# Kernel tuning notes

Hardware: AMD Instinct MI355X
Metric: run time of the kernel (lower is better)

## Reference

```python
import jax, jax.numpy as jnp
import numpy as np

B, T, C = 4, 1024, 768
H, HS = 12, 64           # num_heads, head_size
VD = 2 * HS              # value dim per head


def setup_inputs() -> dict:
    key = jax.random.key(0)
    ks = jax.random.split(key, 16)
    s = 0.02
    inp = {
        "x": jax.random.normal(ks[0], (B, T, C), jnp.float32),
        "Wq1": jax.random.normal(ks[1], (H, C, HS), jnp.float32) * s,
        "Wk1": jax.random.normal(ks[2], (H, C, HS), jnp.float32) * s,
        "Wq2": jax.random.normal(ks[3], (H, C, HS), jnp.float32) * s,
        "Wk2": jax.random.normal(ks[4], (H, C, HS), jnp.float32) * s,
        "Wv": jax.random.normal(ks[5], (H, C, VD), jnp.float32) * s,
        "lq1": jax.random.normal(ks[6], (H, HS), jnp.float32) * 0.1,
        "lk1": jax.random.normal(ks[7], (H, HS), jnp.float32) * 0.1,
        "lq2": jax.random.normal(ks[8], (H, HS), jnp.float32) * 0.1,
        "lk2": jax.random.normal(ks[9], (H, HS), jnp.float32) * 0.1,
        "gn_w": jnp.ones((H * VD,), jnp.float32),
        "gn_b": jnp.zeros((H * VD,), jnp.float32),
        "Wp": jax.random.normal(ks[10], (C, H * VD), jnp.float32) * s,
        "bp": jnp.zeros((C,), jnp.float32),
        "layer_idx": 3,
    }
    return inp


def _diff_attn(x, Wq1, Wk1, Wq2, Wk2, Wv, lq1, lk1, lq2, lk2,
               gn_w, gn_b, Wp, bp, layer_idx):
    Bc, Tc, _ = x.shape
    scale = 1.0 / jnp.sqrt(jnp.float32(HS))
    # per-head projections: [B,H,T,HS]
    q1 = jnp.einsum('btc,hcd->bhtd', x, Wq1)
    k1 = jnp.einsum('btc,hcd->bhtd', x, Wk1)
    q2 = jnp.einsum('btc,hcd->bhtd', x, Wq2)
    k2 = jnp.einsum('btc,hcd->bhtd', x, Wk2)
    v = jnp.einsum('btc,hce->bhte', x, Wv)           # [B,H,T,2HS]
    mask = jnp.tril(jnp.ones((Tc, Tc), bool))         # causal
    neg = jnp.float32(-jnp.inf)
    a1 = jnp.einsum('bhtd,bhsd->bhts', q1, k1) * scale
    a2 = jnp.einsum('bhtd,bhsd->bhts', q2, k2) * scale
    a1 = jax.nn.softmax(jnp.where(mask, a1, neg), axis=-1)
    a2 = jax.nn.softmax(jnp.where(mask, a2, neg), axis=-1)
    # dynamic lambda init, per get_lambda
    li = jnp.float32(layer_idx)
    dyn = 0.8 - 0.6 * jnp.exp(-0.3 * (li - 1.0))
    lam = jnp.mean(jnp.exp(lq1 * lk1) - jnp.exp(lq2 * lk2) + dyn, axis=-1)  # [H]
    diff = a1 - lam[None, :, None, None] * a2
    out = jnp.einsum('bhts,bhse->bhte', diff, v)      # [B,H,T,2HS]
    out = out.transpose(0, 2, 1, 3).reshape(Bc, Tc, H * VD)
    # GroupLayerNorm == full layernorm over last dim (unbiased=False var)
    mu = out.mean(-1, keepdims=True)
    var = jnp.mean((out - mu) ** 2, axis=-1, keepdims=True)
    out = (out - mu) / jnp.sqrt(var + 1e-5) * gn_w + gn_b
    out = out * 0.2  # (1 - lambda_init_buffer=0.8), buffer never updated
    return out @ Wp.T + bp


def reference(x, Wq1, Wk1, Wq2, Wk2, Wv, lq1, lk1, lq2, lk2,
              gn_w, gn_b, Wp, bp, layer_idx):
    return _diff_attn(x, Wq1, Wk1, Wq2, Wk2, Wv, lq1, lk1, lq2, lk2,
                      gn_w, gn_b, Wp, bp, layer_idx)
```

## Files before the change

### kernel.cpp

```cpp
#include <hip/hip_runtime.h>
#include <hip/hip_bf16.h>

#define Bc   4
#define Tc   1024
#define Cc   768
#define Hc   12
#define HSc  64
#define VDc  128
#define NQKV 4608
#define YLD  3072
#define NROWS 4096
#define HVD  1536

#define Q1OFF 0
#define K1OFF 768
#define Q2OFF 1536
#define K2OFF 2304

typedef __bf16 bf16x8 __attribute__((ext_vector_type(8)));
typedef float f32x4 __attribute__((ext_vector_type(4)));
typedef unsigned int u32x4 __attribute__((ext_vector_type(4)));

#define EXP2SCALE 0.18033688011112042f

static __device__ __forceinline__ float bf2f(unsigned short s) {
    return __uint_as_float(((unsigned int)s) << 16);
}
static __device__ __forceinline__ unsigned short f2bf(float f) {
    unsigned int u = __float_as_uint(f);
    unsigned int r = (u + 0x7FFFu + ((u >> 16) & 1u)) >> 16;
    return (unsigned short)r;
}
static __device__ __forceinline__ unsigned int pack2bf(float lo, float hi) {
    unsigned int a = (__float_as_uint(lo) + 0x8000u) >> 16;
    unsigned int b = (__float_as_uint(hi) + 0x8000u) & 0xFFFF0000u;
    return a | b;
}
static __device__ __forceinline__ float fast_exp2(float x) {
    float r;
    asm("v_exp_f32 %0, %1" : "=v"(r) : "v"(x));
    return r;
}

static __device__ __forceinline__ void load16_lds(const void* g, void* l) {
    __builtin_amdgcn_global_load_lds(
        (const __attribute__((address_space(1))) void*)g,
        (__attribute__((address_space(3))) void*)l, 16, 0, 0);
}

__global__ __launch_bounds__(256) void cast_bf16(
    const float* __restrict__ src, unsigned short* __restrict__ dst)
{
    int i = blockIdx.x * 256 + threadIdx.x;
    float4 v = *(const float4*)(src + (size_t)i * 4);
    ushort4 u;
    u.x = f2bf(v.x); u.y = f2bf(v.y); u.z = f2bf(v.z); u.w = f2bf(v.w);
    *(ushort4*)(dst + (size_t)i * 4) = u;
}

__global__ __launch_bounds__(256) void trans_w(
    const float* __restrict__ Wq1, const float* __restrict__ Wk1,
    const float* __restrict__ Wq2, const float* __restrict__ Wk2,
    const float* __restrict__ Wv, unsigned short* __restrict__ WcatT)
{
    __shared__ float tile[64][65];
    int tid = threadIdx.x;
    int t = blockIdx.x;
    int kt = t % 12, nt = t / 12;
    int k0 = kt * 64, n0 = nt * 64;
    const float* src;
    int stride;
    if (n0 < 3072) {
        int which = n0 / 768, m = n0 - which * 768, h = m >> 6;
        const float* W = (which == 0) ? Wq1 : (which == 1) ? Wk1 : (which == 2) ? Wq2 : Wk2;
        src = W + ((size_t)h * 768 + k0) * 64;
        stride = 64;
    } else {
        int rel = n0 - 3072, h = rel >> 7, e0 = rel & 127;
        src = Wv + ((size_t)h * 768 + k0) * 128 + e0;
        stride = 128;
    }
    for (int i = tid; i < 4096; i += 256) {
        int kl = i >> 6, dl = i & 63;
        tile[dl][kl] = src[(size_t)kl * stride + dl];
    }
    __syncthreads();
    for (int i = tid; i < 4096; i += 256) {
        int nl = i >> 6, kl = i & 63;
        WcatT[(size_t)(n0 + nl) * 768 + k0 + kl] = f2bf(tile[nl][kl]);
    }
}

__global__ __launch_bounds__(64) void lambda_kernel(
    const float* __restrict__ lq1, const float* __restrict__ lk1,
    const float* __restrict__ lq2, const float* __restrict__ lk2,
    const int* __restrict__ layer_idx, float* __restrict__ lam)
{
    int h = blockIdx.x, l = threadIdx.x;
    float li = (float)layer_idx[0];
    float dyn = 0.8f - 0.6f * expf(-0.3f * (li - 1.0f));
    int i = h * HSc + l;
    float v = expf(lq1[i] * lk1[i]) - expf(lq2[i] * lk2[i]) + dyn;
    #pragma unroll
    for (int off = 32; off; off >>= 1) v += __shfl_xor(v, off);
    if (l == 0) lam[h] = v * (1.0f / 64.0f);
}

template<int TN, int KD, int LDC, bool OUT_BIAS, bool SPLITV>
__global__ __launch_bounds__(256) void gemm_mfma(
    const unsigned short* __restrict__ A, const unsigned short* __restrict__ Bt,
    unsigned short* __restrict__ Cb, float* __restrict__ Cf,
    const float* __restrict__ bias, unsigned short* __restrict__ VtOut)
{
    constexpr int BN = TN * 32;
    constexpr int JB = TN / 2;
    __shared__ unsigned short As[128 * 32];
    __shared__ unsigned short Bs[BN * 32];
    int tid = threadIdx.x, lane = tid & 63, w = tid >> 6;
    int wm = w >> 1, wn = w & 1;
    int m0 = blockIdx.y * 128, n0 = blockIdx.x * BN;

    int lr = lane >> 2, lq = lane & 3;
    const unsigned short* gA[2];
    const unsigned short* gB[JB];
    #pragma unroll
    for (int j = 0; j < 2; ++j) {
        int row = w * 32 + j * 16 + lr;
        int qg = lq ^ ((row >> 1) & 3);
        gA[j] = A + (size_t)(m0 + row) * KD + qg * 8;
    }
    #pragma unroll
    for (int j = 0; j < JB; ++j) {
        int row = w * (JB * 16) + j * 16 + lr;
        int qg = lq ^ ((row >> 1) & 3);
        gB[j] = Bt + (size_t)(n0 + row) * KD + qg * 8;
    }

    int rr = lane & 15, qd = lane >> 4;
    const unsigned short* aAddr[4];
    const unsigned short* bAddr[TN];
    #pragma unroll
    for (int i = 0; i < 4; ++i) {
        int row = wm * 64 + i * 16 + rr;
        int qs = qd ^ ((row >> 1) & 3);
        aAddr[i] = As + row * 32 + qs * 8;
    }
    #pragma unroll
    for (int t = 0; t < TN; ++t) {
        int row = wn * (TN * 16) + t * 16 + rr;
        int qs = qd ^ ((row >> 1) & 3);
        bAddr[t] = Bs + row * 32 + qs * 8;
    }

    f32x4 acc[4][TN];
    #pragma unroll
    for (int i = 0; i < 4; ++i)
        #pragma unroll
        for (int t = 0; t < TN; ++t) acc[i][t] = {0.f, 0.f, 0.f, 0.f};

    for (int k = 0; k < KD / 32; ++k) {
        __syncthreads();
        load16_lds(gA[0], As + (w * 2 + 0) * 512);
        load16_lds(gA[1], As + (w * 2 + 1) * 512);
        #pragma unroll
        for (int j = 0; j < JB; ++j)
            load16_lds(gB[j], Bs + (w * JB + j) * 512);
        gA[0] += 32; gA[1] += 32;
        #pragma unroll
        for (int j = 0; j < JB; ++j) gB[j] += 32;
        __syncthreads();

        bf16x8 af[4], bfr[TN];
        #pragma unroll
        for (int i = 0; i < 4; ++i) af[i] = *(const bf16x8*)aAddr[i];
        #pragma unroll
        for (int t = 0; t < TN; ++t) bfr[t] = *(const bf16x8*)bAddr[t];
        #pragma unroll
        for (int i = 0; i < 4; ++i)
            #pragma unroll
            for (int t = 0; t < TN; ++t)
                acc[i][t] = __builtin_amdgcn_mfma_f32_16x16x32_bf16(af[i], bfr[t], acc[i][t], 0, 0, 0);
    }

    #pragma unroll
    for (int t = 0; t < TN; ++t) {
        int col = n0 + wn * (TN * 16) + t * 16 + rr;
        if (SPLITV && col >= 3072) {
            int rel = col - 3072, hh = rel >> 7, e = rel & 127;
            #pragma unroll
            for (int i = 0; i < 4; ++i) {
                int row0 = m0 + wm * 64 + i * 16 + qd * 4;
                int b = row0 >> 10, tt = row0 & 1023;
                ushort4 pk;
                pk.x = f2bf(acc[i][t][0]); pk.y = f2bf(acc[i][t][1]);
                pk.z = f2bf(acc[i][t][2]); pk.w = f2bf(acc[i][t][3]);
                *(ushort4*)&VtOut[(size_t)((b * Hc + hh) * 128 + e) * 1024 + tt] = pk;
            }
        } else {
            float bv = OUT_BIAS ? bias[col] : 0.f;
            #pragma unroll
            for (int i = 0; i < 4; ++i) {
                #pragma unroll
                for (int r = 0; r < 4; ++r) {
                    int row = m0 + wm * 64 + i * 16 + qd * 4 + r;
                    if (OUT_BIAS)
                        Cf[(size_t)row * LDC + col] = acc[i][t][r] + bv;
                    else
                        Cb[(size_t)row * LDC + col] = f2bf(acc[i][t][r]);
                }
            }
        }
    }
}

__global__ __launch_bounds__(256) void diff_attn_mfma(
    const unsigned short* __restrict__ Y, const unsigned short* __restrict__ Vt,
    const float* __restrict__ lam_buf, unsigned short* __restrict__ attn)
{
    __shared__ __align__(16) unsigned short KVring[3 * 8192];

    int bh = blockIdx.x;
    int b = bh / Hc, h = bh - b * Hc;
    int g = 15 - (int)blockIdx.y;
    int tid = threadIdx.x, lane = tid & 63, wv = tid >> 6;
    int cl = lane & 15, qd = lane >> 4;
    float lamv = lam_buf[h];
    size_t rowbase = (size_t)(b * Tc) * YLD;
    const int hq = h * HSc;
    const unsigned short* VtB = Vt + ((size_t)bh << 17);
    const f32x4 zero4 = {0.f, 0.f, 0.f, 0.f};

    int ksrow = lane >> 3;
    int ksch  = (lane & 7) ^ ksrow;
    int offk[4];
    {
        int mat = wv & 1;
        int moff = mat ? K2OFF : K1OFF;
        #pragma unroll
        for (int r8 = 0; r8 < 4; ++r8)
            offk[r8] = (r8 * 8 + ksrow) * YLD + moff + hq + ksch * 8;
    }
    int vsel = lane >> 2;
    int vsch = (lane & 3) ^ ((vsel >> 1) & 3);
    int offv[4];
    {
        int sv0 = (wv & 1) * 4;
        #pragma unroll
        for (int i = 0; i < 4; ++i)
            offv[i] = ((sv0 + i) * 16 + vsel) * 1024 + vsch * 8;
    }

    auto stage = [&](int kt, int slot) {
        char* base = (char*)KVring + slot * 16384 + wv * 4096;
        if (wv < 2) {
            const unsigned short* g0 = Y + rowbase + (size_t)(kt * 32) * YLD;
            #pragma unroll
            for (int r8 = 0; r8 < 4; ++r8)
                load16_lds(g0 + offk[r8], base + r8 * 1024);
        } else {
            const unsigned short* g0 = VtB + kt * 32;
            #pragma unroll
            for (int i = 0; i < 4; ++i)
                load16_lds(g0 + offv[i], base + i * 1024);
        }
    };

    int kfo[2][4], vfo[8];
    #pragma unroll
    for (int c = 0; c < 2; ++c) {
        int row = c * 16 + cl;
        #pragma unroll
        for (int j = 0; j < 4; ++j)
            kfo[c][j] = (j >> 1) * 4096 + row * 128 +
                        ((((j & 1) * 4 + qd) ^ (row & 7)) << 4);
    }
    #pragma unroll
    for (int ec = 0; ec < 8; ++ec) {
        int e = ec * 16 + cl;
        vfo[ec] = 8192 + e * 64 + ((qd ^ ((e >> 1) & 3)) << 4);
    }

    int idxA = ((32 * (qd & 1)) + cl) * 4;
    int idxB = idxA + 64;
    bool loHalf = (qd < 2);

    int qrow = g * 64 + wv * 16;

    size_t qoff = rowbase + (size_t)(qrow + cl) * YLD;
    u32x4 uq1a = *(const u32x4*)(Y + qoff + Q1OFF + hq + qd * 8);
    u32x4 uq1b = *(const u32x4*)(Y + qoff + Q1OFF + hq + 32 + qd * 8);
    u32x4 uq2a = *(const u32x4*)(Y + qoff + Q2OFF + hq + qd * 8);
    u32x4 uq2b = *(const u32x4*)(Y + qoff + Q2OFF + hq + 32 + qd * 8);
    asm volatile("" : "+v"(uq1a), "+v"(uq1b), "+v"(uq2a), "+v"(uq2b));
    asm volatile("" : "+v"(lamv));
    asm volatile("s_waitcnt vmcnt(0)" ::: "memory");
    bf16x8 q1a = __builtin_bit_cast(bf16x8, uq1a);
    bf16x8 q1b = __builtin_bit_cast(bf16x8, uq1b);
    bf16x8 q2a = __builtin_bit_cast(bf16x8, uq2a);
    bf16x8 q2b = __builtin_bit_cast(bf16x8, uq2b);

    f32x4 O1[8], O2[8];
    #pragma unroll
    for (int ec = 0; ec < 8; ++ec) { O1[ec] = zero4; O2[ec] = zero4; }
    float l1s = 0.f, l2s = 0.f;

    int NT = 2 * g + 2;
    int ktmax = 2 * g + (wv >> 1);

    stage(0, 0);
    stage(1, 1);

    int cur = 0;
    for (int kt = 0; kt < NT; ++kt) {
        if (kt < NT - 1) {
            asm volatile("s_waitcnt vmcnt(4)\n\ts_barrier" ::: "memory");
        } else {
            asm volatile("s_waitcnt vmcnt(0)\n\ts_barrier" ::: "memory");
        }
        const char* kb = (const char*)KVring + cur * 16384;

        bf16x8 kf[2][4];
        #pragma unroll
        for (int c = 0; c < 2; ++c)
            #pragma unroll
            for (int j = 0; j < 4; ++j)
                kf[c][j] = *(const bf16x8*)(kb + kfo[c][j]);
        bf16x8 vf[8];
        #pragma unroll
        for (int ec = 0; ec < 8; ++ec)
            vf[ec] = *(const bf16x8*)(kb + vfo[ec]);

        if (kt + 2 < NT) {
            int st = cur + 2; if (st >= 3) st -= 3;
            stage(kt + 2, st);
        }

        if (kt <= ktmax) {
            f32x4 S1[2], S2[2];
            #pragma unroll
            for (int c = 0; c < 2; ++c) { S1[c] = zero4; S2[c] = zero4; }
            #pragma unroll
            for (int c = 0; c < 2; ++c) {
                S1[c] = __builtin_amdgcn_mfma_f32_16x16x32_bf16(kf[c][0], q1a, S1[c], 0, 0, 0);
                S1[c] = __builtin_amdgcn_mfma_f32_16x16x32_bf16(kf[c][1], q1b, S1[c], 0, 0, 0);
                S2[c] = __builtin_amdgcn_mfma_f32_16x16x32_bf16(kf[c][2], q2a, S2[c], 0, 0, 0);
                S2[c] = __builtin_amdgcn_mfma_f32_16x16x32_bf16(kf[c][3], q2b, S2[c], 0, 0, 0);
            }
            if (kt * 32 + 31 > qrow) {
                #pragma unroll
                for (int c = 0; c < 2; ++c) {
                    int lim = qrow + cl - kt * 32 - c * 16 - qd * 4;
                    #pragma unroll
                    for (int r = 0; r < 4; ++r) {
                        if (r > lim) { S1[c][r] = -1e30f; S2[c][r] = -1e30f; }
                    }
                }
            }
            float p1v[2][4], p2v[2][4];
            #pragma unroll
            for (int c = 0; c < 2; ++c) {
                #pragma unroll
                for (int r = 0; r < 4; ++r) {
                    p1v[c][r] = fast_exp2(S1[c][r] * EXP2SCALE);
                    p2v[c][r] = fast_exp2(S2[c][r] * EXP2SCALE);
                    l1s += p1v[c][r];
                    l2s += p2v[c][r];
                }
            }
            unsigned int s1m[2][2], s2m[2][2];
            #pragma unroll
            for (int c = 0; c < 2; ++c) {
                s1m[c][0] = pack2bf(p1v[c][0], p1v[c][1]);
                s1m[c][1] = pack2bf(p1v[c][2], p1v[c][3]);
                s2m[c][0] = pack2bf(p2v[c][0], p2v[c][1]);
                s2m[c][1] = pack2bf(p2v[c][2], p2v[c][3]);
            }
            u32x4 U1, U2;
            {
                int a00 = __builtin_amdgcn_ds_bpermute(idxA, (int)s1m[0][0]);
                int a10 = __builtin_amdgcn_ds_bpermute(idxA, (int)s1m[1][0]);
                int a01 = __builtin_amdgcn_ds_bpermute(idxA, (int)s1m[0][1]);
                int a11 = __builtin_amdgcn_ds_bpermute(idxA, (int)s1m[1][1]);
                int b00 = __builtin_amdgcn_ds_bpermute(idxB, (int)s1m[0][0]);
                int b10 = __builtin_amdgcn_ds_bpermute(idxB, (int)s1m[1][0]);
                int b01 = __builtin_amdgcn_ds_bpermute(idxB, (int)s1m[0][1]);
                int b11 = __builtin_amdgcn_ds_bpermute(idxB, (int)s1m[1][1]);
                U1[0] = (unsigned)(loHalf ? a00 : a10);
                U1[1] = (unsigned)(loHalf ? a01 : a11);
                U1[2] = (unsigned)(loHalf ? b00 : b10);
                U1[3] = (unsigned)(loHalf ? b01 : b11);
            }
            {
                int a00 = __builtin_amdgcn_ds_bpermute(idxA, (int)s2m[0][0]);
                int a10 = __builtin_amdgcn_ds_bpermute(idxA, (int)s2m[1][0]);
                int a01 = __builtin_amdgcn_ds_bpermute(idxA, (int)s2m[0][1]);
                int a11 = __builtin_amdgcn_ds_bpermute(idxA, (int)s2m[1][1]);
                int b00 = __builtin_amdgcn_ds_bpermute(idxB, (int)s2m[0][0]);
                int b10 = __builtin_amdgcn_ds_bpermute(idxB, (int)s2m[1][0]);
                int b01 = __builtin_amdgcn_ds_bpermute(idxB, (int)s2m[0][1]);
                int b11 = __builtin_amdgcn_ds_bpermute(idxB, (int)s2m[1][1]);
                U2[0] = (unsigned)(loHalf ? a00 : a10);
                U2[1] = (unsigned)(loHalf ? a01 : a11);
                U2[2] = (unsigned)(loHalf ? b00 : b10);
                U2[3] = (unsigned)(loHalf ? b01 : b11);
            }
            bf16x8 pa1 = __builtin_bit_cast(bf16x8, U1);
            bf16x8 pa2 = __builtin_bit_cast(bf16x8, U2);
            #pragma unroll
            for (int ec = 0; ec < 8; ++ec) {
                O1[ec] = __builtin_amdgcn_mfma_f32_16x16x32_bf16(pa1, vf[ec], O1[ec], 0, 0, 0);
                O2[ec] = __builtin_amdgcn_mfma_f32_16x16x32_bf16(pa2, vf[ec], O2[ec], 0, 0, 0);
            }
        }
        cur = (cur == 2) ? 0 : cur + 1;
    }

    l1s += __shfl_xor(l1s, 16); l1s += __shfl_xor(l1s, 32);
    l2s += __shfl_xor(l2s, 16); l2s += __shfl_xor(l2s, 32);
    float w1[4], w2[4];
    #pragma unroll
    for (int r = 0; r < 4; ++r) {
        float d1 = __shfl(l1s, qd * 4 + r);
        float d2 = __shfl(l2s, qd * 4 + r);
        w1[r] = 1.0f / d1;
        w2[r] = lamv / d2;
    }
    #pragma unroll
    for (int ec = 0; ec < 8; ++ec) {
        #pragma unroll
        for (int r = 0; r < 4; ++r) {
            size_t row = (size_t)(b * Tc + qrow + qd * 4 + r);
            attn[row * HVD + h * VDc + ec * 16 + cl] =
                f2bf(O1[ec][r] * w1[r] - O2[ec][r] * w2[r]);
        }
    }
}

__global__ __launch_bounds__(128) void ln_inplace(
    unsigned short* __restrict__ attn,
    const float* __restrict__ gnw, const float* __restrict__ gnb)
{
    int row = blockIdx.x, tid = threadIdx.x;
    unsigned short* p = attn + (size_t)row * HVD;
    float v[12];
    float s = 0.f, sq = 0.f;
    #pragma unroll
    for (int j = 0; j < 3; ++j) {
        int g = tid + j * 128;
        ushort4 u = *(const ushort4*)(p + g * 4);
        float x0 = bf2f(u.x), x1 = bf2f(u.y), x2 = bf2f(u.z), x3 = bf2f(u.w);
        v[j * 4 + 0] = x0; v[j * 4 + 1] = x1; v[j * 4 + 2] = x2; v[j * 4 + 3] = x3;
        s += x0 + x1 + x2 + x3;
        sq = fmaf(x0, x0, sq); sq = fmaf(x1, x1, sq);
        sq = fmaf(x2, x2, sq); sq = fmaf(x3, x3, sq);
    }
    #pragma unroll
    for (int off = 32; off; off >>= 1) { s += __shfl_xor(s, off); sq += __shfl_xor(sq, off); }
    __shared__ float ss[2], sqs[2];
    if ((tid & 63) == 0) { ss[tid >> 6] = s; sqs[tid >> 6] = sq; }
    __syncthreads();
    float S = ss[0] + ss[1], Q = sqs[0] + sqs[1];
    float mu = S * (1.0f / HVD);
    float rstd = rsqrtf(Q * (1.0f / HVD) - mu * mu + 1e-5f);
    #pragma unroll
    for (int j = 0; j < 3; ++j) {
        int g = tid + j * 128;
        float4 gw = *(const float4*)(gnw + g * 4);
        float4 gb = *(const float4*)(gnb + g * 4);
        ushort4 o;
        o.x = f2bf(((v[j * 4 + 0] - mu) * rstd * gw.x + gb.x) * 0.2f);
        o.y = f2bf(((v[j * 4 + 1] - mu) * rstd * gw.y + gb.y) * 0.2f);
        o.z = f2bf(((v[j * 4 + 2] - mu) * rstd * gw.z + gb.z) * 0.2f);
        o.w = f2bf(((v[j * 4 + 3] - mu) * rstd * gw.w + gb.w) * 0.2f);
        *(ushort4*)(p + g * 4) = o;
    }
}

extern "C" void kernel_launch(void* const* d_in, const int* in_sizes, int n_in,
                              void* d_out, int out_size, void* d_ws, size_t ws_size,
                              hipStream_t stream)
{
    const float* x   = (const float*)d_in[0];
    const float* Wq1 = (const float*)d_in[1];
    const float* Wk1 = (const float*)d_in[2];
    const float* Wq2 = (const float*)d_in[3];
    const float* Wk2 = (const float*)d_in[4];
    const float* Wv  = (const float*)d_in[5];
    const float* lq1 = (const float*)d_in[6];
    const float* lk1 = (const float*)d_in[7];
    const float* lq2 = (const float*)d_in[8];
    const float* lk2 = (const float*)d_in[9];
    const float* gnw = (const float*)d_in[10];
    const float* gnb = (const float*)d_in[11];
    const float* Wp  = (const float*)d_in[12];
    const float* bp  = (const float*)d_in[13];
    const int*   lidx = (const int*)d_in[14];
    float* out = (float*)d_out;

    char* w = (char*)d_ws;
    unsigned short* WcatT = (unsigned short*)(w);
    unsigned short* Xb    = (unsigned short*)(w + 7077888);
    unsigned short* Y     = (unsigned short*)(w + 13369344);
    unsigned short* VtW   = (unsigned short*)(w + 38535168);
    unsigned short* attn  = (unsigned short*)(w + 51118080);
    unsigned short* Wpb   = (unsigned short*)(w + 63700992);
    float* lam            = (float*)(w + 66060288);

    cast_bf16<<<dim3(NROWS * Cc / 1024), 256, 0, stream>>>(x, Xb);
    cast_bf16<<<dim3(Cc * HVD / 1024), 256, 0, stream>>>(Wp, Wpb);
    trans_w<<<dim3(72 * 12), 256, 0, stream>>>(Wq1, Wk1, Wq2, Wk2, Wv, WcatT);
    lambda_kernel<<<dim3(Hc), 64, 0, stream>>>(lq1, lk1, lq2, lk2, lidx, lam);
    gemm_mfma<4, 768, YLD, false, true><<<dim3(NQKV / 128, NROWS / 128), 256, 0, stream>>>(
        Xb, WcatT, Y, nullptr, nullptr, VtW);
    diff_attn_mfma<<<dim3(Bc * Hc, 16), 256, 0, stream>>>(Y, VtW, lam, attn);
    ln_inplace<<<dim3(NROWS), 128, 0, stream>>>(attn, gnw, gnb);
    gemm_mfma<2, HVD, Cc, true, false><<<dim3(Cc / 64, NROWS / 128), 256, 0, stream>>>(
        attn, Wpb, nullptr, out, bp, nullptr);
}
```

Before: 274.4 us.

## Process two key tiles per iteration with a double-buffered 64-key LDS stage

The attention kernel's K/V staging goes from a three-slot ring of 32-key tiles to two 32 KB slots. Each slot holds two 32-key tiles, with waves split by parity to stage them. Each loop iteration now computes scores and PV products for 64 keys after a single barrier, so there are half as many barriers and more independent MFMA work to interleave. The costs are a full vmcnt(0) wait each iteration, which gives less prefetch depth than the old ring, more LDS per block (64 KB vs 48 KB) that may reduce occupancy, and a dropped per-wave skip of the fully masked last tile.

```diff
diff --git a/kernel.cpp b/kernel.cpp
--- a/kernel.cpp
+++ b/kernel.cpp
@@ -217,7 +217,7 @@
     const unsigned short* __restrict__ Y, const unsigned short* __restrict__ Vt,
     const float* __restrict__ lam_buf, unsigned short* __restrict__ attn)
 {
-    __shared__ __align__(16) unsigned short KVring[3 * 8192];
+    __shared__ __align__(16) unsigned short KVring[2 * 16384];
 
     int bh = blockIdx.x;
     int b = bh / Hc, h = bh - b * Hc;
@@ -230,39 +230,36 @@
     const unsigned short* VtB = Vt + ((size_t)bh << 17);
     const f32x4 zero4 = {0.f, 0.f, 0.f, 0.f};
 
-    int ksrow = lane >> 3;
-    int ksch  = (lane & 7) ^ ksrow;
-    int offk[4];
-    {
-        int mat = wv & 1;
-        int moff = mat ? K2OFF : K1OFF;
-        #pragma unroll
-        for (int r8 = 0; r8 < 4; ++r8)
-            offk[r8] = (r8 * 8 + ksrow) * YLD + moff + hq + ksch * 8;
-    }
-    int vsel = lane >> 2;
-    int vsch = (lane & 3) ^ ((vsel >> 1) & 3);
-    int offv[4];
-    {
-        int sv0 = (wv & 1) * 4;
-        #pragma unroll
-        for (int i = 0; i < 4; ++i)
-            offv[i] = ((sv0 + i) * 16 + vsel) * 1024 + vsch * 8;
-    }
-
-    auto stage = [&](int kt, int slot) {
-        char* base = (char*)KVring + slot * 16384 + wv * 4096;
-        if (wv < 2) {
-            const unsigned short* g0 = Y + rowbase + (size_t)(kt * 32) * YLD;
-            #pragma unroll
-            for (int r8 = 0; r8 < 4; ++r8)
-                load16_lds(g0 + offk[r8], base + r8 * 1024);
-        } else {
-            const unsigned short* g0 = VtB + kt * 32;
-            #pragma unroll
-            for (int i = 0; i < 4; ++i)
-                load16_lds(g0 + offv[i], base + i * 1024);
-        }
+    int sub = wv & 1;
+    int off8[8];
+    int dstoff;
+    if (wv < 2) {
+        int ksrow = lane >> 3;
+        int ksch  = (lane & 7) ^ ksrow;
+        #pragma unroll
+        for (int j = 0; j < 8; ++j) {
+            int moff = (j < 4) ? K1OFF : K2OFF;
+            off8[j] = ((j & 3) * 8 + ksrow) * YLD + moff + hq + ksch * 8;
+        }
+        dstoff = 0;
+    } else {
+        int vsel = lane >> 2;
+        int vsch = (lane & 3) ^ ((vsel >> 1) & 3);
+        #pragma unroll
+        for (int s = 0; s < 8; ++s)
+            off8[s] = (s * 16 + vsel) * 1024 + vsch * 8;
+        dstoff = 8192;
+    }
+
+    auto stage = [&](int i, int slot) {
+        int kt = 2 * i + sub;
+        char* base = (char*)KVring + slot * 32768 + sub * 16384 + dstoff;
+        const unsigned short* g0 = (wv < 2)
+            ? (Y + rowbase + (size_t)(kt * 32) * YLD)
+            : (VtB + kt * 32);
+        #pragma unroll
+        for (int j = 0; j < 8; ++j)
+            load16_lds(g0 + off8[j], base + j * 1024);
     };
 
     int kfo[2][4], vfo[8];
@@ -286,133 +283,138 @@
 
     int qrow = g * 64 + wv * 16;
 
+    stage(0, 0);
+
     size_t qoff = rowbase + (size_t)(qrow + cl) * YLD;
-    u32x4 uq1a = *(const u32x4*)(Y + qoff + Q1OFF + hq + qd * 8);
-    u32x4 uq1b = *(const u32x4*)(Y + qoff + Q1OFF + hq + 32 + qd * 8);
-    u32x4 uq2a = *(const u32x4*)(Y + qoff + Q2OFF + hq + qd * 8);
-    u32x4 uq2b = *(const u32x4*)(Y + qoff + Q2OFF + hq + 32 + qd * 8);
-    asm volatile("" : "+v"(uq1a), "+v"(uq1b), "+v"(uq2a), "+v"(uq2b));
-    asm volatile("" : "+v"(lamv));
-    asm volatile("s_waitcnt vmcnt(0)" ::: "memory");
-    bf16x8 q1a = __builtin_bit_cast(bf16x8, uq1a);
-    bf16x8 q1b = __builtin_bit_cast(bf16x8, uq1b);
-    bf16x8 q2a = __builtin_bit_cast(bf16x8, uq2a);
-    bf16x8 q2b = __builtin_bit_cast(bf16x8, uq2b);
+    bf16x8 q1a = *(const bf16x8*)(Y + qoff + Q1OFF + hq + qd * 8);
+    bf16x8 q1b = *(const bf16x8*)(Y + qoff + Q1OFF + hq + 32 + qd * 8);
+    bf16x8 q2a = *(const bf16x8*)(Y + qoff + Q2OFF + hq + qd * 8);
+    bf16x8 q2b = *(const bf16x8*)(Y + qoff + Q2OFF + hq + 32 + qd * 8);
 
     f32x4 O1[8], O2[8];
     #pragma unroll
     for (int ec = 0; ec < 8; ++ec) { O1[ec] = zero4; O2[ec] = zero4; }
     float l1s = 0.f, l2s = 0.f;
 
-    int NT = 2 * g + 2;
-    int ktmax = 2 * g + (wv >> 1);
-
-    stage(0, 0);
-    stage(1, 1);
-
-    int cur = 0;
-    for (int kt = 0; kt < NT; ++kt) {
-        if (kt < NT - 1) {
-            asm volatile("s_waitcnt vmcnt(4)\n\ts_barrier" ::: "memory");
-        } else {
-            asm volatile("s_waitcnt vmcnt(0)\n\ts_barrier" ::: "memory");
-        }
-        const char* kb = (const char*)KVring + cur * 16384;
-
-        bf16x8 kf[2][4];
+    auto transform = [&](f32x4 S1[2], f32x4 S2[2], int kt,
+                         bf16x8& pa1o, bf16x8& pa2o) {
+        if (kt * 32 + 31 > qrow) {
+            #pragma unroll
+            for (int c = 0; c < 2; ++c) {
+                int lim = qrow + cl - kt * 32 - c * 16 - qd * 4;
+                #pragma unroll
+                for (int r = 0; r < 4; ++r) {
+                    if (r > lim) { S1[c][r] = -1e30f; S2[c][r] = -1e30f; }
+                }
+            }
+        }
+        float p1v[2][4], p2v[2][4];
+        #pragma unroll
+        for (int c = 0; c < 2; ++c) {
+            #pragma unroll
+            for (int r = 0; r < 4; ++r) {
+                p1v[c][r] = fast_exp2(S1[c][r] * EXP2SCALE);
+                p2v[c][r] = fast_exp2(S2[c][r] * EXP2SCALE);
+                l1s += p1v[c][r];
+                l2s += p2v[c][r];
+            }
+        }
+        unsigned int s1m[2][2], s2m[2][2];
+        #pragma unroll
+        for (int c = 0; c < 2; ++c) {
+            s1m[c][0] = pack2bf(p1v[c][0], p1v[c][1]);
+            s1m[c][1] = pack2bf(p1v[c][2], p1v[c][3]);
+            s2m[c][0] = pack2bf(p2v[c][0], p2v[c][1]);
+            s2m[c][1] = pack2bf(p2v[c][2], p2v[c][3]);
+        }
+        u32x4 U1, U2;
+        {
+            int a00 = __builtin_amdgcn_ds_bpermute(idxA, (int)s1m[0][0]);
+            int a10 = __builtin_amdgcn_ds_bpermute(idxA, (int)s1m[1][0]);
+            int a01 = __builtin_amdgcn_ds_bpermute(idxA, (int)s1m[0][1]);
+            int a11 = __builtin_amdgcn_ds_bpermute(idxA, (int)s1m[1][1]);
+            int b00 = __builtin_amdgcn_ds_bpermute(idxB, (int)s1m[0][0]);
+            int b10 = __builtin_amdgcn_ds_bpermute(idxB, (int)s1m[1][0]);
+            int b01 = __builtin_amdgcn_ds_bpermute(idxB, (int)s1m[0][1]);
+            int b11 = __builtin_amdgcn_ds_bpermute(idxB, (int)s1m[1][1]);
+            U1[0] = (unsigned)(loHalf ? a00 : a10);
+            U1[1] = (unsigned)(loHalf ? a01 : a11);
+            U1[2] = (unsigned)(loHalf ? b00 : b10);
+            U1[3] = (unsigned)(loHalf ? b01 : b11);
+        }
+        {
+            int a00 = __builtin_amdgcn_ds_bpermute(idxA, (int)s2m[0][0]);
+            int a10 = __builtin_amdgcn_ds_bpermute(idxA, (int)s2m[1][0]);
+            int a01 = __builtin_amdgcn_ds_bpermute(idxA, (int)s2m[0][1]);
+            int a11 = __builtin_amdgcn_ds_bpermute(idxA, (int)s2m[1][1]);
+            int b00 = __builtin_amdgcn_ds_bpermute(idxB, (int)s2m[0][0]);
+            int b10 = __builtin_amdgcn_ds_bpermute(idxB, (int)s2m[1][0]);
+            int b01 = __builtin_amdgcn_ds_bpermute(idxB, (int)s2m[0][1]);
+            int b11 = __builtin_amdgcn_ds_bpermute(idxB, (int)s2m[1][1]);
+            U2[0] = (unsigned)(loHalf ? a00 : a10);
+            U2[1] = (unsigned)(loHalf ? a01 : a11);
+            U2[2] = (unsigned)(loHalf ? b00 : b10);
+            U2[3] = (unsigned)(loHalf ? b01 : b11);
+        }
+        pa1o = __builtin_bit_cast(bf16x8, U1);
+        pa2o = __builtin_bit_cast(bf16x8, U2);
+    };
+
+    int NI = g + 1;
+    for (int i = 0; i < NI; ++i) {
+        asm volatile("s_waitcnt vmcnt(0)\n\ts_barrier" ::: "memory");
+        const char* kbA = (const char*)KVring + (i & 1) * 32768;
+        const char* kbB = kbA + 16384;
+        if (i + 1 < NI) stage(i + 1, (i + 1) & 1);
+
+        bf16x8 kfA[2][4], kfB[2][4];
         #pragma unroll
         for (int c = 0; c < 2; ++c)
             #pragma unroll
-            for (int j = 0; j < 4; ++j)
-                kf[c][j] = *(const bf16x8*)(kb + kfo[c][j]);
-        bf16x8 vf[8];
+            for (int j = 0; j < 4; ++j) {
+                kfA[c][j] = *(const bf16x8*)(kbA + kfo[c][j]);
+                kfB[c][j] = *(const bf16x8*)(kbB + kfo[c][j]);
+            }
+        bf16x8 vfA[8];
         #pragma unroll
         for (int ec = 0; ec < 8; ++ec)
-            vf[ec] = *(const bf16x8*)(kb + vfo[ec]);
-
-        if (kt + 2 < NT) {
-            int st = cur + 2; if (st >= 3) st -= 3;
-            stage(kt + 2, st);
-        }
-
-        if (kt <= ktmax) {
-            f32x4 S1[2], S2[2];
-            #pragma unroll
-            for (int c = 0; c < 2; ++c) { S1[c] = zero4; S2[c] = zero4; }
-            #pragma unroll
-            for (int c = 0; c < 2; ++c) {
-                S1[c] = __builtin_amdgcn_mfma_f32_16x16x32_bf16(kf[c][0], q1a, S1[c], 0, 0, 0);
-                S1[c] = __builtin_amdgcn_mfma_f32_16x16x32_bf16(kf[c][1], q1b, S1[c], 0, 0, 0);
-                S2[c] = __builtin_amdgcn_mfma_f32_16x16x32_bf16(kf[c][2], q2a, S2[c], 0, 0, 0);
-                S2[c] = __builtin_amdgcn_mfma_f32_16x16x32_bf16(kf[c][3], q2b, S2[c], 0, 0, 0);
-            }
-            if (kt * 32 + 31 > qrow) {
-                #pragma unroll
-                for (int c = 0; c < 2; ++c) {
-                    int lim = qrow + cl - kt * 32 - c * 16 - qd * 4;
-                    #pragma unroll
-                    for (int r = 0; r < 4; ++r) {
-                        if (r > lim) { S1[c][r] = -1e30f; S2[c][r] = -1e30f; }
-                    }
-                }
-            }
-            float p1v[2][4], p2v[2][4];
-            #pragma unroll
-            for (int c = 0; c < 2; ++c) {
-                #pragma unroll
-                for (int r = 0; r < 4; ++r) {
-                    p1v[c][r] = fast_exp2(S1[c][r] * EXP2SCALE);
-                    p2v[c][r] = fast_exp2(S2[c][r] * EXP2SCALE);
-                    l1s += p1v[c][r];
-                    l2s += p2v[c][r];
-                }
-            }
-            unsigned int s1m[2][2], s2m[2][2];
-            #pragma unroll
-            for (int c = 0; c < 2; ++c) {
-                s1m[c][0] = pack2bf(p1v[c][0], p1v[c][1]);
-                s1m[c][1] = pack2bf(p1v[c][2], p1v[c][3]);
-                s2m[c][0] = pack2bf(p2v[c][0], p2v[c][1]);
-                s2m[c][1] = pack2bf(p2v[c][2], p2v[c][3]);
-            }
-            u32x4 U1, U2;
-            {
-                int a00 = __builtin_amdgcn_ds_bpermute(idxA, (int)s1m[0][0]);
-                int a10 = __builtin_amdgcn_ds_bpermute(idxA, (int)s1m[1][0]);
-                int a01 = __builtin_amdgcn_ds_bpermute(idxA, (int)s1m[0][1]);
-                int a11 = __builtin_amdgcn_ds_bpermute(idxA, (int)s1m[1][1]);
-                int b00 = __builtin_amdgcn_ds_bpermute(idxB, (int)s1m[0][0]);
-                int b10 = __builtin_amdgcn_ds_bpermute(idxB, (int)s1m[1][0]);
-                int b01 = __builtin_amdgcn_ds_bpermute(idxB, (int)s1m[0][1]);
-                int b11 = __builtin_amdgcn_ds_bpermute(idxB, (int)s1m[1][1]);
-                U1[0] = (unsigned)(loHalf ? a00 : a10);
-                U1[1] = (unsigned)(loHalf ? a01 : a11);
-                U1[2] = (unsigned)(loHalf ? b00 : b10);
-                U1[3] = (unsigned)(loHalf ? b01 : b11);
-            }
-            {
-                int a00 = __builtin_amdgcn_ds_bpermute(idxA, (int)s2m[0][0]);
-                int a10 = __builtin_amdgcn_ds_bpermute(idxA, (int)s2m[1][0]);
-                int a01 = __builtin_amdgcn_ds_bpermute(idxA, (int)s2m[0][1]);
-                int a11 = __builtin_amdgcn_ds_bpermute(idxA, (int)s2m[1][1]);
-                int b00 = __builtin_amdgcn_ds_bpermute(idxB, (int)s2m[0][0]);
-                int b10 = __builtin_amdgcn_ds_bpermute(idxB, (int)s2m[1][0]);
-                int b01 = __builtin_amdgcn_ds_bpermute(idxB, (int)s2m[0][1]);
-                int b11 = __builtin_amdgcn_ds_bpermute(idxB, (int)s2m[1][1]);
-                U2[0] = (unsigned)(loHalf ? a00 : a10);
-                U2[1] = (unsigned)(loHalf ? a01 : a11);
-                U2[2] = (unsigned)(loHalf ? b00 : b10);
-                U2[3] = (unsigned)(loHalf ? b01 : b11);
-            }
-            bf16x8 pa1 = __builtin_bit_cast(bf16x8, U1);
-            bf16x8 pa2 = __builtin_bit_cast(bf16x8, U2);
-            #pragma unroll
-            for (int ec = 0; ec < 8; ++ec) {
-                O1[ec] = __builtin_amdgcn_mfma_f32_16x16x32_bf16(pa1, vf[ec], O1[ec], 0, 0, 0);
-                O2[ec] = __builtin_amdgcn_mfma_f32_16x16x32_bf16(pa2, vf[ec], O2[ec], 0, 0, 0);
-            }
-        }
-        cur = (cur == 2) ? 0 : cur + 1;
+            vfA[ec] = *(const bf16x8*)(kbA + vfo[ec]);
+
+        f32x4 S1A[2], S2A[2], S1B[2], S2B[2];
+        #pragma unroll
+        for (int c = 0; c < 2; ++c) {
+            S1A[c] = zero4; S2A[c] = zero4; S1B[c] = zero4; S2B[c] = zero4;
+        }
+        #pragma unroll
+        for (int c = 0; c < 2; ++c) {
+            S1A[c] = __builtin_amdgcn_mfma_f32_16x16x32_bf16(kfA[c][0], q1a, S1A[c], 0, 0, 0);
+            S1A[c] = __builtin_amdgcn_mfma_f32_16x16x32_bf16(kfA[c][1], q1b, S1A[c], 0, 0, 0);
+            S2A[c] = __builtin_amdgcn_mfma_f32_16x16x32_bf16(kfA[c][2], q2a, S2A[c], 0, 0, 0);
+            S2A[c] = __builtin_amdgcn_mfma_f32_16x16x32_bf16(kfA[c][3], q2b, S2A[c], 0, 0, 0);
+            S1B[c] = __builtin_amdgcn_mfma_f32_16x16x32_bf16(kfB[c][0], q1a, S1B[c], 0, 0, 0);
+            S1B[c] = __builtin_amdgcn_mfma_f32_16x16x32_bf16(kfB[c][1], q1b, S1B[c], 0, 0, 0);
+            S2B[c] = __builtin_amdgcn_mfma_f32_16x16x32_bf16(kfB[c][2], q2a, S2B[c], 0, 0, 0);
+            S2B[c] = __builtin_amdgcn_mfma_f32_16x16x32_bf16(kfB[c][3], q2b, S2B[c], 0, 0, 0);
+        }
+
+        bf16x8 pa1A, pa2A, pa1B, pa2B;
+        transform(S1A, S2A, 2 * i, pa1A, pa2A);
+        bf16x8 vfB[8];
+        #pragma unroll
+        for (int ec = 0; ec < 8; ++ec)
+            vfB[ec] = *(const bf16x8*)(kbB + vfo[ec]);
+        transform(S1B, S2B, 2 * i + 1, pa1B, pa2B);
+
+        #pragma unroll
+        for (int ec = 0; ec < 8; ++ec) {
+            O1[ec] = __builtin_amdgcn_mfma_f32_16x16x32_bf16(pa1A, vfA[ec], O1[ec], 0, 0, 0);
+            O2[ec] = __builtin_amdgcn_mfma_f32_16x16x32_bf16(pa2A, vfA[ec], O2[ec], 0, 0, 0);
+        }
+        #pragma unroll
+        for (int ec = 0; ec < 8; ++ec) {
+            O1[ec] = __builtin_amdgcn_mfma_f32_16x16x32_bf16(pa1B, vfB[ec], O1[ec], 0, 0, 0);
+            O2[ec] = __builtin_amdgcn_mfma_f32_16x16x32_bf16(pa2B, vfB[ec], O2[ec], 0, 0, 0);
+        }
     }
 
     l1s += __shfl_xor(l1s, 16); l1s += __shfl_xor(l1s, 32);
```

Measured after the change: 250.9 us. 1.09x faster.
